# Kernel optimization log

Hardware: AMD Instinct MI355X
Metric: run time of the kernel (lower is better)

The kernel has to match this reference:

```python
import jax, jax.numpy as jnp
import numpy as np

EPS = 1e-06
TEMPERATURE = 1.0
RATIO_WEIGHT = 1.0
ENTROPY_WEIGHT = 0.01


def setup_inputs() -> dict:
    key = jax.random.key(0)
    k1, k2, k3 = jax.random.split(key, 3)
    B, N, C, H = 32, 4096, 256, 256
    x = jax.random.normal(k1, (B, N, C), dtype=jnp.float32)
    W1 = jax.random.normal(k2, (C, H), dtype=jnp.float32) * (1.0 / np.sqrt(C))
    b1 = jnp.zeros((H,), dtype=jnp.float32)
    w2 = jax.random.normal(k3, (H,), dtype=jnp.float32) * (1.0 / np.sqrt(H))
    b2 = jnp.zeros((1,), dtype=jnp.float32)
    return {"x": x, "W1": W1, "b1": b1, "w2": w2, "b2": b2, "k": 16}


def reference(x, W1, b1, w2, b2, k):
    # x: [B, N, C] -> soft-mode TokenGater forward
    N = x.shape[-2]
    # MLP scorer: Linear -> GELU(exact) -> Linear -> squeeze(-1)
    h = jax.nn.gelu(jnp.einsum('bnc,ch->bnh', x, W1) + b1, approximate=False)
    scores = jnp.einsum('bnh,h->bn', h, w2) + b2[0]              # [B, N]
    probs = jax.nn.sigmoid(scores / max(TEMPERATURE, EPS))       # [B, N]

    target_ratio = float(k) / float(max(N, 1))
    ratio = probs.mean(axis=-1)                                  # [B]
    loss_ratio = jnp.mean((ratio - target_ratio) ** 2)
    loss_entropy = jnp.mean(-(probs * jnp.log(probs + EPS)
                              + (1.0 - probs) * jnp.log(1.0 - probs + EPS)))
    aux_loss = RATIO_WEIGHT * loss_ratio + ENTROPY_WEIGHT * loss_entropy

    x_keep = x * probs[..., None]                                # [B, N, C]
    bg_w = 1.0 - probs                                           # [B, N]
    denom = jnp.clip(bg_w.sum(axis=-1, keepdims=True), EPS)      # [B, 1]
    bg = jnp.einsum('bnc,bn->bc', x, bg_w) / denom               # [B, C]
    y = jnp.concatenate([x_keep, bg[..., None, :]], axis=-2)     # [B, N+1, C]
    return (y, aux_loss, scores, probs)
```

## Files before the change

kernel.cpp:

```cpp
#include <hip/hip_runtime.h>
#include <cstdint>

#define GEPS 1e-6f

typedef __attribute__((ext_vector_type(8))) short bf16x8;
typedef __attribute__((ext_vector_type(4))) float f32x4;

__device__ __forceinline__ unsigned short f2bf(float f) {
  unsigned int u = __float_as_uint(f);
  u += 0x7fffu + ((u >> 16) & 1u);
  return (unsigned short)(u >> 16);
}

__global__ void pack_w1(const float* __restrict__ W1, unsigned short* __restrict__ wt) {
  int k = blockIdx.x;
  int h = threadIdx.x;
  float v = W1[k * 256 + h];
  int h_tile = h >> 4, tl = h & 15, kk = k >> 5, q = (k >> 3) & 3, j = k & 7;
  wt[(((h_tile << 3) + kk) << 9) + (q << 7) + (tl << 3) + j] = f2bf(v);
}

__global__ __launch_bounds__(256) void gater_main(
    const float* __restrict__ x, const unsigned short* __restrict__ wt,
    const float* __restrict__ b1, const float* __restrict__ w2,
    const float* __restrict__ b2,
    float* __restrict__ y, float* __restrict__ scores, float* __restrict__ probs,
    float* __restrict__ bg_ws, float* __restrict__ sums)
{
  __shared__ short A_lds[64 * 264];
  __shared__ float sc_lds[4][64];
  __shared__ float p_lds[64];
  __shared__ float bg_lds[4][256];

  const int tid = threadIdx.x;
  const int tok0 = blockIdx.x * 64;
  const int b = tok0 >> 12;
  const int n0 = tok0 & 4095;
  const float* xblk = x + (size_t)tok0 * 256;

  #pragma unroll
  for (int i = 0; i < 16; ++i) {
    int f = i * 256 + tid;
    int token = f >> 6;
    int k4 = (f & 63) << 2;
    const float4 v = *(const float4*)(xblk + (size_t)f * 4);
    unsigned int lo = (unsigned int)f2bf(v.x) | ((unsigned int)f2bf(v.y) << 16);
    unsigned int hi = (unsigned int)f2bf(v.z) | ((unsigned int)f2bf(v.w) << 16);
    *(uint2*)&A_lds[token * 264 + k4] = make_uint2(lo, hi);
  }
  __syncthreads();

  const int wave = tid >> 6, lane = tid & 63, tl = lane & 15, q = lane >> 4;

  f32x4 acc[4][4];
  #pragma unroll
  for (int mi = 0; mi < 4; ++mi)
    #pragma unroll
    for (int ni = 0; ni < 4; ++ni)
      acc[mi][ni] = (f32x4){0.f, 0.f, 0.f, 0.f};

  const bf16x8* wtv = (const bf16x8*)wt;
  #pragma unroll
  for (int kk = 0; kk < 8; ++kk) {
    bf16x8 a[4], bb[4];
    #pragma unroll
    for (int mi = 0; mi < 4; ++mi)
      a[mi] = *(const bf16x8*)&A_lds[(mi * 16 + tl) * 264 + kk * 32 + q * 8];
    #pragma unroll
    for (int ni = 0; ni < 4; ++ni)
      bb[ni] = wtv[((((wave << 2) + ni) << 3) + kk) * 64 + lane];
    #pragma unroll
    for (int mi = 0; mi < 4; ++mi)
      #pragma unroll
      for (int ni = 0; ni < 4; ++ni)
        acc[mi][ni] = __builtin_amdgcn_mfma_f32_16x16x32_bf16(a[mi], bb[ni], acc[mi][ni], 0, 0, 0);
  }

  float w2v[4], b1v[4];
  #pragma unroll
  for (int ni = 0; ni < 4; ++ni) {
    int h = wave * 64 + ni * 16 + tl;
    w2v[ni] = w2[h];
    b1v[ni] = b1[h];
  }
  #pragma unroll
  for (int mi = 0; mi < 4; ++mi) {
    #pragma unroll
    for (int r = 0; r < 4; ++r) {
      float s = 0.f;
      #pragma unroll
      for (int ni = 0; ni < 4; ++ni) {
        float hv = acc[mi][ni][r] + b1v[ni];
        float g = 0.5f * hv * (1.0f + erff(hv * 0.70710678118654752f));
        s += g * w2v[ni];
      }
      #pragma unroll
      for (int m = 1; m < 16; m <<= 1) s += __shfl_xor(s, m, 64);
      if (tl == 0) sc_lds[wave][mi * 16 + q * 4 + r] = s;
    }
  }
  __syncthreads();

  if (tid < 64) {
    float s = sc_lds[0][tid] + sc_lds[1][tid] + sc_lds[2][tid] + sc_lds[3][tid] + b2[0];
    float p = 1.0f / (1.0f + expf(-s));
    size_t g = (size_t)tok0 + tid;
    scores[g] = s;
    probs[g] = p;
    p_lds[tid] = p;
    float ent = -(p * logf(p + GEPS) + (1.0f - p) * logf(1.0f - p + GEPS));
    float sp = p, se = ent;
    #pragma unroll
    for (int m = 1; m < 64; m <<= 1) {
      sp += __shfl_xor(sp, m, 64);
      se += __shfl_xor(se, m, 64);
    }
    if (tid == 0) {
      atomicAdd(&sums[b * 2 + 0], sp);
      atomicAdd(&sums[b * 2 + 1], se);
    }
  }
  __syncthreads();

  float4 bg = make_float4(0.f, 0.f, 0.f, 0.f);
  #pragma unroll
  for (int i = 0; i < 16; ++i) {
    int f = i * 256 + tid;
    int token = f >> 6;
    float4 xv = *(const float4*)(xblk + (size_t)f * 4);
    float p = p_lds[token];
    float4 yv = make_float4(xv.x * p, xv.y * p, xv.z * p, xv.w * p);
    size_t row = (size_t)b * 4097 + (size_t)(n0 + token);
    *(float4*)(y + row * 256 + ((f & 63) << 2)) = yv;
    float bw = 1.0f - p;
    bg.x += xv.x * bw; bg.y += xv.y * bw; bg.z += xv.z * bw; bg.w += xv.w * bw;
  }
  *(float4*)&bg_lds[tid >> 6][(tid & 63) << 2] = bg;
  __syncthreads();
  {
    int c = tid;
    float v = bg_lds[0][c] + bg_lds[1][c] + bg_lds[2][c] + bg_lds[3][c];
    atomicAdd(&bg_ws[b * 256 + c], v);
  }
}

__global__ void finalize(const float* __restrict__ bg_ws, const float* __restrict__ sums,
                         const int* __restrict__ kp, float* __restrict__ y,
                         float* __restrict__ aux)
{
  int b = blockIdx.x, c = threadIdx.x;
  float sp = sums[b * 2 + 0];
  float denom = fmaxf(4096.0f - sp, GEPS);
  y[((size_t)b * 4097 + 4096) * 256 + c] = bg_ws[b * 256 + c] / denom;
  if (b == 0 && c == 0) {
    float t = (float)kp[0] / 4096.0f;
    float lr = 0.f, le = 0.f;
    for (int i = 0; i < 32; ++i) {
      float r = sums[i * 2 + 0] / 4096.0f;
      lr += (r - t) * (r - t);
      le += sums[i * 2 + 1];
    }
    aux[0] = lr / 32.0f + 0.01f * (le / (32.0f * 4096.0f));
  }
}

extern "C" void kernel_launch(void* const* d_in, const int* in_sizes, int n_in,
                              void* d_out, int out_size, void* d_ws, size_t ws_size,
                              hipStream_t stream) {
  const float* x  = (const float*)d_in[0];
  const float* W1 = (const float*)d_in[1];
  const float* b1 = (const float*)d_in[2];
  const float* w2 = (const float*)d_in[3];
  const float* b2 = (const float*)d_in[4];
  const int*   kp = (const int*)d_in[5];

  float* y = (float*)d_out;
  const size_t Y_ELEMS = (size_t)32 * 4097 * 256;
  float* aux    = y + Y_ELEMS;
  float* scores = aux + 1;
  float* probs  = scores + (size_t)32 * 4096;

  unsigned short* wt = (unsigned short*)d_ws;
  float* bg_ws = (float*)((char*)d_ws + 131072);
  float* sums  = bg_ws + 32 * 256;

  hipMemsetAsync(bg_ws, 0, (32 * 256 + 64) * sizeof(float), stream);
  pack_w1<<<256, 256, 0, stream>>>(W1, wt);
  gater_main<<<2048, 256, 0, stream>>>(x, wt, b1, w2, b2, y, scores, probs, bg_ws, sums);
  finalize<<<32, 256, 0, stream>>>(bg_ws, sums, kp, y, aux);
}
```

Measured before the change: 311.5 us.

## Reuse bf16 LDS copy of x for output, retile to 32 tokens, fast math

The second pass now rebuilds x from the bf16 copy already staged in LDS instead of re-reading the fp32 input from global memory. This removes a full second read of x. The price is that y and the background sum are computed from bf16-rounded x, so they lose precision. The block is retiled to 32 tokens with 128 threads (two waves, each covering 128 hidden units), with occupancy hints. Exact erf, exp and log are replaced by a polynomial erf approximation and hardware exp2/rcp/log intrinsics.

Result: slower. 355.5 us (+14.1%).

```diff
diff --git a/kernel.cpp b/kernel.cpp
--- a/kernel.cpp
+++ b/kernel.cpp
@@ -10,6 +10,30 @@
   unsigned int u = __float_as_uint(f);
   u += 0x7fffu + ((u >> 16) & 1u);
   return (unsigned short)(u >> 16);
+}
+
+__device__ __forceinline__ float bf2f(unsigned short h) {
+  return __uint_as_float(((unsigned int)h) << 16);
+}
+
+__device__ __forceinline__ float fast_gelu(float x) {
+  float z  = x * 0.70710678118654752f;
+  float az = fabsf(z);
+  float t  = __builtin_amdgcn_rcpf(fmaf(0.3275911f, az, 1.0f));
+  float poly = t * fmaf(t, fmaf(t, fmaf(t, fmaf(t, 1.061405429f, -1.453152027f),
+                    1.421413741f), -0.284496736f), 0.254829592f);
+  float e  = __builtin_amdgcn_exp2f(-az * az * 1.4426950408889634f);
+  float ea = fmaf(-poly, e, 1.0f);
+  float er = __uint_as_float(__float_as_uint(ea) | (__float_as_uint(z) & 0x80000000u));
+  return 0.5f * x * (1.0f + er);
+}
+
+__device__ __forceinline__ float fast_sigmoid(float s) {
+  return __builtin_amdgcn_rcpf(1.0f + __builtin_amdgcn_exp2f(-s * 1.4426950408889634f));
+}
+
+__device__ __forceinline__ float fast_log(float x) {
+  return __builtin_amdgcn_logf(x) * 0.69314718055994531f;
 }
 
 __global__ void pack_w1(const float* __restrict__ W1, unsigned short* __restrict__ wt) {
@@ -20,80 +44,75 @@
   wt[(((h_tile << 3) + kk) << 9) + (q << 7) + (tl << 3) + j] = f2bf(v);
 }
 
-__global__ __launch_bounds__(256) void gater_main(
+__global__ __launch_bounds__(128, 4) void gater_main(
     const float* __restrict__ x, const unsigned short* __restrict__ wt,
     const float* __restrict__ b1, const float* __restrict__ w2,
     const float* __restrict__ b2,
     float* __restrict__ y, float* __restrict__ scores, float* __restrict__ probs,
     float* __restrict__ bg_ws, float* __restrict__ sums)
 {
-  __shared__ short A_lds[64 * 264];
-  __shared__ float sc_lds[4][64];
-  __shared__ float p_lds[64];
-  __shared__ float bg_lds[4][256];
+  __shared__ short A_lds[32 * 260];
+  __shared__ float sc_lds[2][32];
+  __shared__ float p_lds[32];
+  __shared__ float bg_lds[2][256];
 
   const int tid = threadIdx.x;
-  const int tok0 = blockIdx.x * 64;
+  const int tok0 = blockIdx.x * 32;
   const int b = tok0 >> 12;
   const int n0 = tok0 & 4095;
   const float* xblk = x + (size_t)tok0 * 256;
 
   #pragma unroll
   for (int i = 0; i < 16; ++i) {
-    int f = i * 256 + tid;
+    int f = i * 128 + tid;
     int token = f >> 6;
     int k4 = (f & 63) << 2;
     const float4 v = *(const float4*)(xblk + (size_t)f * 4);
     unsigned int lo = (unsigned int)f2bf(v.x) | ((unsigned int)f2bf(v.y) << 16);
     unsigned int hi = (unsigned int)f2bf(v.z) | ((unsigned int)f2bf(v.w) << 16);
-    *(uint2*)&A_lds[token * 264 + k4] = make_uint2(lo, hi);
+    *(uint2*)&A_lds[token * 260 + k4] = make_uint2(lo, hi);
   }
   __syncthreads();
 
   const int wave = tid >> 6, lane = tid & 63, tl = lane & 15, q = lane >> 4;
 
-  f32x4 acc[4][4];
-  #pragma unroll
-  for (int mi = 0; mi < 4; ++mi)
-    #pragma unroll
-    for (int ni = 0; ni < 4; ++ni)
+  f32x4 acc[2][8];
+  #pragma unroll
+  for (int mi = 0; mi < 2; ++mi)
+    #pragma unroll
+    for (int ni = 0; ni < 8; ++ni)
       acc[mi][ni] = (f32x4){0.f, 0.f, 0.f, 0.f};
 
   const bf16x8* wtv = (const bf16x8*)wt;
   #pragma unroll
   for (int kk = 0; kk < 8; ++kk) {
-    bf16x8 a[4], bb[4];
-    #pragma unroll
-    for (int mi = 0; mi < 4; ++mi)
-      a[mi] = *(const bf16x8*)&A_lds[(mi * 16 + tl) * 264 + kk * 32 + q * 8];
-    #pragma unroll
-    for (int ni = 0; ni < 4; ++ni)
-      bb[ni] = wtv[((((wave << 2) + ni) << 3) + kk) * 64 + lane];
-    #pragma unroll
-    for (int mi = 0; mi < 4; ++mi)
-      #pragma unroll
-      for (int ni = 0; ni < 4; ++ni)
-        acc[mi][ni] = __builtin_amdgcn_mfma_f32_16x16x32_bf16(a[mi], bb[ni], acc[mi][ni], 0, 0, 0);
-  }
-
-  float w2v[4], b1v[4];
-  #pragma unroll
-  for (int ni = 0; ni < 4; ++ni) {
-    int h = wave * 64 + ni * 16 + tl;
+    bf16x8 a[2];
+    #pragma unroll
+    for (int mi = 0; mi < 2; ++mi)
+      a[mi] = *(const bf16x8*)&A_lds[(mi * 16 + tl) * 260 + kk * 32 + q * 8];
+    #pragma unroll
+    for (int ni = 0; ni < 8; ++ni) {
+      bf16x8 bb = wtv[(((wave * 8 + ni) * 8) + kk) * 64 + lane];
+      acc[0][ni] = __builtin_amdgcn_mfma_f32_16x16x32_bf16(a[0], bb, acc[0][ni], 0, 0, 0);
+      acc[1][ni] = __builtin_amdgcn_mfma_f32_16x16x32_bf16(a[1], bb, acc[1][ni], 0, 0, 0);
+    }
+  }
+
+  float w2v[8], b1v[8];
+  #pragma unroll
+  for (int ni = 0; ni < 8; ++ni) {
+    int h = wave * 128 + ni * 16 + tl;
     w2v[ni] = w2[h];
     b1v[ni] = b1[h];
   }
   #pragma unroll
-  for (int mi = 0; mi < 4; ++mi) {
+  for (int mi = 0; mi < 2; ++mi) {
     #pragma unroll
     for (int r = 0; r < 4; ++r) {
       float s = 0.f;
       #pragma unroll
-      for (int ni = 0; ni < 4; ++ni) {
-        float hv = acc[mi][ni][r] + b1v[ni];
-        float g = 0.5f * hv * (1.0f + erff(hv * 0.70710678118654752f));
-        s += g * w2v[ni];
-      }
+      for (int ni = 0; ni < 8; ++ni)
+        s += fast_gelu(acc[mi][ni][r] + b1v[ni]) * w2v[ni];
       #pragma unroll
       for (int m = 1; m < 16; m <<= 1) s += __shfl_xor(s, m, 64);
       if (tl == 0) sc_lds[wave][mi * 16 + q * 4 + r] = s;
@@ -101,17 +120,17 @@
   }
   __syncthreads();
 
-  if (tid < 64) {
-    float s = sc_lds[0][tid] + sc_lds[1][tid] + sc_lds[2][tid] + sc_lds[3][tid] + b2[0];
-    float p = 1.0f / (1.0f + expf(-s));
+  if (tid < 32) {
+    float s = sc_lds[0][tid] + sc_lds[1][tid] + b2[0];
+    float p = fast_sigmoid(s);
     size_t g = (size_t)tok0 + tid;
     scores[g] = s;
     probs[g] = p;
     p_lds[tid] = p;
-    float ent = -(p * logf(p + GEPS) + (1.0f - p) * logf(1.0f - p + GEPS));
+    float ent = -(p * fast_log(p + GEPS) + (1.0f - p) * fast_log(1.0f - p + GEPS));
     float sp = p, se = ent;
     #pragma unroll
-    for (int m = 1; m < 64; m <<= 1) {
+    for (int m = 1; m < 32; m <<= 1) {
       sp += __shfl_xor(sp, m, 64);
       se += __shfl_xor(se, m, 64);
     }
@@ -125,22 +144,31 @@
   float4 bg = make_float4(0.f, 0.f, 0.f, 0.f);
   #pragma unroll
   for (int i = 0; i < 16; ++i) {
-    int f = i * 256 + tid;
+    int f = i * 128 + tid;
     int token = f >> 6;
-    float4 xv = *(const float4*)(xblk + (size_t)f * 4);
+    int k4 = (f & 63) << 2;
+    uint2 raw = *(const uint2*)&A_lds[token * 260 + k4];
+    float4 xv = make_float4(bf2f((unsigned short)(raw.x & 0xffffu)),
+                            bf2f((unsigned short)(raw.x >> 16)),
+                            bf2f((unsigned short)(raw.y & 0xffffu)),
+                            bf2f((unsigned short)(raw.y >> 16)));
     float p = p_lds[token];
-    float4 yv = make_float4(xv.x * p, xv.y * p, xv.z * p, xv.w * p);
     size_t row = (size_t)b * 4097 + (size_t)(n0 + token);
-    *(float4*)(y + row * 256 + ((f & 63) << 2)) = yv;
+    *(float4*)(y + row * 256 + k4) =
+        make_float4(xv.x * p, xv.y * p, xv.z * p, xv.w * p);
     float bw = 1.0f - p;
     bg.x += xv.x * bw; bg.y += xv.y * bw; bg.z += xv.z * bw; bg.w += xv.w * bw;
   }
   *(float4*)&bg_lds[tid >> 6][(tid & 63) << 2] = bg;
   __syncthreads();
-  {
-    int c = tid;
-    float v = bg_lds[0][c] + bg_lds[1][c] + bg_lds[2][c] + bg_lds[3][c];
-    atomicAdd(&bg_ws[b * 256 + c], v);
+  if (tid < 64) {
+    int c = tid << 2;
+    float4 v0 = *(const float4*)&bg_lds[0][c];
+    float4 v1 = *(const float4*)&bg_lds[1][c];
+    atomicAdd(&bg_ws[b * 256 + c + 0], v0.x + v1.x);
+    atomicAdd(&bg_ws[b * 256 + c + 1], v0.y + v1.y);
+    atomicAdd(&bg_ws[b * 256 + c + 2], v0.z + v1.z);
+    atomicAdd(&bg_ws[b * 256 + c + 3], v0.w + v1.w);
   }
 }
 
@@ -186,6 +214,6 @@
 
   hipMemsetAsync(bg_ws, 0, (32 * 256 + 64) * sizeof(float), stream);
   pack_w1<<<256, 256, 0, stream>>>(W1, wt);
-  gater_main<<<2048, 256, 0, stream>>>(x, wt, b1, w2, b2, y, scores, probs, bg_ws, sums);
+  gater_main<<<4096, 128, 0, stream>>>(x, wt, b1, w2, b2, y, scores, probs, bg_ws, sums);
   finalize<<<32, 256, 0, stream>>>(bg_ws, sums, kp, y, aux);
 }
```

## Split gater into score and apply kernels with fast GELU and sigmoid

Applied to the files above, without the earlier changes.

Splits the fused kernel into a scoring kernel (MFMA MLP plus sigmoid and loss sums) and a separate streaming apply kernel that scales x, writes y with nontemporal stores, and writes per-chunk background partials instead of using atomics. Replaces erf-based GELU, expf and logf with polynomial and hardware exp2, rcp and log approximations. It also vectorizes the W1 packing and batches x loads before the bf16 conversion. The trade-off is a second full pass over x, plus slightly reduced accuracy from the approximate GELU.

New measurement: 315.1 us. No clear change (+1.2%).

```diff
diff --git a/kernel.cpp b/kernel.cpp
--- a/kernel.cpp
+++ b/kernel.cpp
@@ -12,41 +12,72 @@
   return (unsigned short)(u >> 16);
 }
 
-__global__ void pack_w1(const float* __restrict__ W1, unsigned short* __restrict__ wt) {
-  int k = blockIdx.x;
-  int h = threadIdx.x;
-  float v = W1[k * 256 + h];
-  int h_tile = h >> 4, tl = h & 15, kk = k >> 5, q = (k >> 3) & 3, j = k & 7;
-  wt[(((h_tile << 3) + kk) << 9) + (q << 7) + (tl << 3) + j] = f2bf(v);
-}
-
-__global__ __launch_bounds__(256) void gater_main(
+__device__ __forceinline__ float fast_gelu(float x) {
+  float z  = x * 0.70710678118654752f;
+  float az = fabsf(z);
+  float t  = __builtin_amdgcn_rcpf(fmaf(0.3275911f, az, 1.0f));
+  float poly = t * fmaf(t, fmaf(t, fmaf(t, fmaf(t, 1.061405429f, -1.453152027f),
+                    1.421413741f), -0.284496736f), 0.254829592f);
+  float e  = __builtin_amdgcn_exp2f(-az * az * 1.4426950408889634f);
+  float ea = fmaf(-poly, e, 1.0f);
+  float er = __uint_as_float(__float_as_uint(ea) | (__float_as_uint(z) & 0x80000000u));
+  return 0.5f * x * (1.0f + er);
+}
+
+__device__ __forceinline__ float fast_sigmoid(float s) {
+  return __builtin_amdgcn_rcpf(1.0f + __builtin_amdgcn_exp2f(-s * 1.4426950408889634f));
+}
+
+__device__ __forceinline__ float fast_log(float x) {
+  return __builtin_amdgcn_logf(x) * 0.69314718055994531f;
+}
+
+__global__ __launch_bounds__(256) void pack_w1(const float* __restrict__ W1,
+                                               unsigned short* __restrict__ wt) {
+  int t = blockIdx.x * 256 + threadIdx.x;
+  int frag = t >> 6, l = t & 63;
+  int ht = frag >> 3, kk = frag & 7, q = l >> 4, tl = l & 15;
+  int h = ht * 16 + tl, k0 = kk * 32 + q * 8;
+  unsigned int w[4];
+  #pragma unroll
+  for (int jj = 0; jj < 4; ++jj) {
+    unsigned short lo = f2bf(W1[(k0 + 2 * jj) * 256 + h]);
+    unsigned short hi = f2bf(W1[(k0 + 2 * jj + 1) * 256 + h]);
+    w[jj] = (unsigned int)lo | ((unsigned int)hi << 16);
+  }
+  uint4* dst = (uint4*)(wt + (size_t)frag * 512 + l * 8);
+  *dst = make_uint4(w[0], w[1], w[2], w[3]);
+}
+
+__global__ __launch_bounds__(256) void score_kernel(
     const float* __restrict__ x, const unsigned short* __restrict__ wt,
     const float* __restrict__ b1, const float* __restrict__ w2,
     const float* __restrict__ b2,
-    float* __restrict__ y, float* __restrict__ scores, float* __restrict__ probs,
-    float* __restrict__ bg_ws, float* __restrict__ sums)
+    float* __restrict__ scores, float* __restrict__ probs, float* __restrict__ sums)
 {
-  __shared__ short A_lds[64 * 264];
+  __shared__ short A_lds[64 * 260];
   __shared__ float sc_lds[4][64];
-  __shared__ float p_lds[64];
-  __shared__ float bg_lds[4][256];
 
   const int tid = threadIdx.x;
   const int tok0 = blockIdx.x * 64;
   const int b = tok0 >> 12;
-  const int n0 = tok0 & 4095;
   const float* xblk = x + (size_t)tok0 * 256;
 
   #pragma unroll
-  for (int i = 0; i < 16; ++i) {
-    int f = i * 256 + tid;
-    int token = f >> 6;
-    int k4 = (f & 63) << 2;
-    const float4 v = *(const float4*)(xblk + (size_t)f * 4);
-    unsigned int lo = (unsigned int)f2bf(v.x) | ((unsigned int)f2bf(v.y) << 16);
-    unsigned int hi = (unsigned int)f2bf(v.z) | ((unsigned int)f2bf(v.w) << 16);
-    *(uint2*)&A_lds[token * 264 + k4] = make_uint2(lo, hi);
+  for (int half = 0; half < 2; ++half) {
+    float4 v[8];
+    #pragma unroll
+    for (int i = 0; i < 8; ++i)
+      v[i] = *(const float4*)(xblk + (size_t)((half * 8 + i) * 256 + tid) * 4);
+    #pragma unroll
+    for (int i = 0; i < 8; ++i) {
+      int f = (half * 8 + i) * 256 + tid;
+      int token = f >> 6;
+      int k4 = (f & 63) << 2;
+      unsigned int lo = (unsigned int)f2bf(v[i].x) | ((unsigned int)f2bf(v[i].y) << 16);
+      unsigned int hi = (unsigned int)f2bf(v[i].z) | ((unsigned int)f2bf(v[i].w) << 16);
+      *(uint2*)&A_lds[token * 260 + k4] = make_uint2(lo, hi);
+    }
   }
   __syncthreads();
 
@@ -65,7 +96,7 @@
     bf16x8 a[4], bb[4];
     #pragma unroll
     for (int mi = 0; mi < 4; ++mi)
-      a[mi] = *(const bf16x8*)&A_lds[(mi * 16 + tl) * 264 + kk * 32 + q * 8];
+      a[mi] = *(const bf16x8*)&A_lds[(mi * 16 + tl) * 260 + kk * 32 + q * 8];
     #pragma unroll
     for (int ni = 0; ni < 4; ++ni)
       bb[ni] = wtv[((((wave << 2) + ni) << 3) + kk) * 64 + lane];
@@ -89,11 +120,8 @@
     for (int r = 0; r < 4; ++r) {
       float s = 0.f;
       #pragma unroll
-      for (int ni = 0; ni < 4; ++ni) {
-        float hv = acc[mi][ni][r] + b1v[ni];
-        float g = 0.5f * hv * (1.0f + erff(hv * 0.70710678118654752f));
-        s += g * w2v[ni];
-      }
+      for (int ni = 0; ni < 4; ++ni)
+        s += fast_gelu(acc[mi][ni][r] + b1v[ni]) * w2v[ni];
       #pragma unroll
       for (int m = 1; m < 16; m <<= 1) s += __shfl_xor(s, m, 64);
       if (tl == 0) sc_lds[wave][mi * 16 + q * 4 + r] = s;
@@ -103,12 +131,11 @@
 
   if (tid < 64) {
     float s = sc_lds[0][tid] + sc_lds[1][tid] + sc_lds[2][tid] + sc_lds[3][tid] + b2[0];
-    float p = 1.0f / (1.0f + expf(-s));
+    float p = fast_sigmoid(s);
     size_t g = (size_t)tok0 + tid;
     scores[g] = s;
     probs[g] = p;
-    p_lds[tid] = p;
-    float ent = -(p * logf(p + GEPS) + (1.0f - p) * logf(1.0f - p + GEPS));
+    float ent = -(p * fast_log(p + GEPS) + (1.0f - p) * fast_log(1.0f - p + GEPS));
     float sp = p, se = ent;
     #pragma unroll
     for (int m = 1; m < 64; m <<= 1) {
@@ -120,38 +147,62 @@
       atomicAdd(&sums[b * 2 + 1], se);
     }
   }
+}
+
+__global__ __launch_bounds__(256) void apply_kernel(
+    const float* __restrict__ x, const float* __restrict__ probs,
+    float* __restrict__ y, float* __restrict__ bg_scratch)
+{
+  __shared__ float p_lds[128];
+  __shared__ float bg_lds[4][256];
+
+  const int tid = threadIdx.x;
+  const int b = blockIdx.x >> 5;
+  const int chunk = blockIdx.x & 31;
+  const float* xb = x + ((size_t)b * 4096 + chunk * 128) * 256;
+  float* yb = y + ((size_t)b * 4097 + chunk * 128) * 256;
+
+  if (tid < 128) p_lds[tid] = probs[b * 4096 + chunk * 128 + tid];
   __syncthreads();
 
   float4 bg = make_float4(0.f, 0.f, 0.f, 0.f);
-  #pragma unroll
-  for (int i = 0; i < 16; ++i) {
-    int f = i * 256 + tid;
+  #pragma unroll 4
+  for (int it = 0; it < 32; ++it) {
+    int f = it * 256 + tid;
     int token = f >> 6;
-    float4 xv = *(const float4*)(xblk + (size_t)f * 4);
+    float4 xv = *(const float4*)(xb + (size_t)f * 4);
     float p = p_lds[token];
-    float4 yv = make_float4(xv.x * p, xv.y * p, xv.z * p, xv.w * p);
-    size_t row = (size_t)b * 4097 + (size_t)(n0 + token);
-    *(float4*)(y + row * 256 + ((f & 63) << 2)) = yv;
+    f32x4 yv = {xv.x * p, xv.y * p, xv.z * p, xv.w * p};
+    __builtin_nontemporal_store(yv, (f32x4*)(yb + (size_t)f * 4));
     float bw = 1.0f - p;
     bg.x += xv.x * bw; bg.y += xv.y * bw; bg.z += xv.z * bw; bg.w += xv.w * bw;
   }
   *(float4*)&bg_lds[tid >> 6][(tid & 63) << 2] = bg;
   __syncthreads();
-  {
-    int c = tid;
-    float v = bg_lds[0][c] + bg_lds[1][c] + bg_lds[2][c] + bg_lds[3][c];
-    atomicAdd(&bg_ws[b * 256 + c], v);
-  }
-}
-
-__global__ void finalize(const float* __restrict__ bg_ws, const float* __restrict__ sums,
-                         const int* __restrict__ kp, float* __restrict__ y,
-                         float* __restrict__ aux)
+  if (tid < 64) {
+    int c = tid << 2;
+    float4 v0 = *(const float4*)&bg_lds[0][c];
+    float4 v1 = *(const float4*)&bg_lds[1][c];
+    float4 v2 = *(const float4*)&bg_lds[2][c];
+    float4 v3 = *(const float4*)&bg_lds[3][c];
+    float4 r = make_float4(v0.x + v1.x + v2.x + v3.x, v0.y + v1.y + v2.y + v3.y,
+                           v0.z + v1.z + v2.z + v3.z, v0.w + v1.w + v2.w + v3.w);
+    *(float4*)(bg_scratch + (size_t)blockIdx.x * 256 + c) = r;
+  }
+}
+
+__global__ __launch_bounds__(256) void finalize(
+    const float* __restrict__ bg_scratch, const float* __restrict__ sums,
+    const int* __restrict__ kp, float* __restrict__ y, float* __restrict__ aux)
 {
   int b = blockIdx.x, c = threadIdx.x;
+  float s = 0.f;
+  #pragma unroll 8
+  for (int chunk = 0; chunk < 32; ++chunk)
+    s += bg_scratch[((size_t)(b * 32 + chunk)) * 256 + c];
   float sp = sums[b * 2 + 0];
   float denom = fmaxf(4096.0f - sp, GEPS);
-  y[((size_t)b * 4097 + 4096) * 256 + c] = bg_ws[b * 256 + c] / denom;
+  y[((size_t)b * 4097 + 4096) * 256 + c] = s / denom;
   if (b == 0 && c == 0) {
     float t = (float)kp[0] / 4096.0f;
     float lr = 0.f, le = 0.f;
@@ -181,11 +232,12 @@
   float* probs  = scores + (size_t)32 * 4096;
 
   unsigned short* wt = (unsigned short*)d_ws;
-  float* bg_ws = (float*)((char*)d_ws + 131072);
-  float* sums  = bg_ws + 32 * 256;
-
-  hipMemsetAsync(bg_ws, 0, (32 * 256 + 64) * sizeof(float), stream);
-  pack_w1<<<256, 256, 0, stream>>>(W1, wt);
-  gater_main<<<2048, 256, 0, stream>>>(x, wt, b1, w2, b2, y, scores, probs, bg_ws, sums);
-  finalize<<<32, 256, 0, stream>>>(bg_ws, sums, kp, y, aux);
-}
+  float* sums       = (float*)((char*)d_ws + 131072);
+  float* bg_scratch = (float*)((char*)d_ws + 135168);
+
+  hipMemsetAsync(sums, 0, 64 * sizeof(float), stream);
+  pack_w1<<<32, 256, 0, stream>>>(W1, wt);
+  score_kernel<<<2048, 256, 0, stream>>>(x, wt, b1, w2, b2, scores, probs, sums);
+  apply_kernel<<<1024, 256, 0, stream>>>(x, probs, y, bg_scratch);
+  finalize<<<32, 256, 0, stream>>>(bg_scratch, sums, kp, y, aux);
+}
```
